# Performance work log

Measured on AMD Instinct MI355X. Metric: run time of the kernel, lower is better.

## Reference

```python
import jax, jax.numpy as jnp
import numpy as np

N = 16384  # n_nodes
D = 64     # feature dim


def setup_inputs() -> dict:
    key = jax.random.key(0)
    kx, ka = jax.random.split(key)
    x = jax.random.normal(kx, (N, D), dtype=jnp.float32)
    # original code only tests adj[idx] == 1, so 0/1 int entries are faithful
    adj = jax.random.randint(ka, (N, N), 0, 2, dtype=jnp.int32)
    return {"x": x, "adj": adj}


def reference(x, adj):
    # GraphPool: for each node, sum its own feature vector plus the feature
    # vectors of all neighbors j with adj[i, j] == 1.
    # Vectorized: out = adj @ x + x  (dense binary SpMM + self term).
    a = (adj == 1).astype(x.dtype)  # [N, N]
    return jnp.matmul(a, x) + x     # [N, D]
```

## Files before the change

kernel.cpp:

```cpp
#include <hip/hip_runtime.h>

#define NN 16384
#define DD 64

typedef _Float16 f16x8 __attribute__((ext_vector_type(8)));
typedef short    s16x8 __attribute__((ext_vector_type(8)));
typedef float    f32x4 __attribute__((ext_vector_type(4)));
typedef int      i32x4 __attribute__((ext_vector_type(4)));

__global__ __launch_bounds__(256) void prep_x(const float* __restrict__ x,
                                              _Float16* __restrict__ ws) {
    __shared__ float sx[32][65];
    const int tid = threadIdx.x;
    const int t   = blockIdx.x;

    {
        int r  = tid >> 3;
        int c8 = (tid & 7) * 8;
        const float* src = x + ((size_t)t * 32 + r) * DD + c8;
        f32x4 a = *(const f32x4*)src;
        f32x4 b = *(const f32x4*)(src + 4);
#pragma unroll
        for (int j = 0; j < 4; ++j) { sx[r][c8 + j] = a[j]; sx[r][c8 + 4 + j] = b[j]; }
    }
    __syncthreads();

    const int l = tid & 63;
    const int c = tid >> 6;
    const int q = l >> 4;
    const int m = l & 15;
    f16x8 v;
#pragma unroll
    for (int j = 0; j < 8; ++j)
        v[j] = (_Float16)sx[q * 8 + j][c * 16 + m];
    *(f16x8*)(ws + (((size_t)t * 256 + c * 64 + l) * 8)) = v;
}

__global__ __launch_bounds__(256, 3) void graphpool_gemm(const int* __restrict__ adj,
                                                         const _Float16* __restrict__ xs,
                                                         float* __restrict__ part) {
    __shared__ _Float16 sB[2][8192];

    const int tid = threadIdx.x;
    const int w   = tid >> 6;
    const int l   = tid & 63;
    const int q   = l >> 4;
    const int m   = l & 15;

    const int rb    = blockIdx.x >> 2;
    const int kq    = blockIdx.x & 3;
    const int row16 = rb * 64 + w * 16;
    constexpr int KQ  = NN / 4;
    constexpr int NCH = KQ / 128;

    const int* aptr = adj + (size_t)(row16 + m) * NN + (size_t)kq * KQ + q * 8;

    f32x4 acc[4];
#pragma unroll
    for (int c = 0; c < 4; ++c) acc[c] = (f32x4){0.f, 0.f, 0.f, 0.f};

    i32x4 areg[2][4][2];
    f16x8 sreg[4];

    auto loadA = [&](int n, int buf) {
#pragma unroll
        for (int s = 0; s < 4; ++s) {
            const i32x4* p = (const i32x4*)(aptr + (size_t)n * 128 + s * 32);
            areg[buf][s][0] = __builtin_nontemporal_load(p);
            areg[buf][s][1] = __builtin_nontemporal_load(p + 1);
        }
    };
    auto stageRead = [&](int n) {
        const f16x8* src = (const f16x8*)xs + (size_t)kq * 32768 + (size_t)n * 1024;
#pragma unroll
        for (int p = 0; p < 4; ++p) sreg[p] = src[p * 256 + tid];
    };
    auto stageWrite = [&](int buf) {
        f16x8* dst = (f16x8*)sB[buf];
#pragma unroll
        for (int p = 0; p < 4; ++p) dst[p * 256 + tid] = sreg[p];
    };

    stageRead(0);
    loadA(0, 0);
    stageWrite(0);
    __syncthreads();

    for (int n = 0; n < NCH; ++n) {
        const int buf = n & 1;
        const bool pf = (n + 1 < NCH);
        if (pf) { stageRead(n + 1); loadA(n + 1, buf ^ 1); }
#pragma unroll
        for (int s = 0; s < 4; ++s) {
            int av[8];
            {
                i32x4 v0 = areg[buf][s][0], v1 = areg[buf][s][1];
                av[0] = v0.x; av[1] = v0.y; av[2] = v0.z; av[3] = v0.w;
                av[4] = v1.x; av[5] = v1.y; av[6] = v1.z; av[7] = v1.w;
            }
            s16x8 ai;
#pragma unroll
            for (int j = 0; j < 8; ++j)
                ai[j] = av[j] ? (short)0x3C00 : (short)0;
            f16x8 af = __builtin_bit_cast(f16x8, ai);
#pragma unroll
            for (int c = 0; c < 4; ++c) {
                f16x8 bf = *(const f16x8*)&sB[buf][((s * 4 + c) * 64 + l) * 8];
                acc[c] = __builtin_amdgcn_mfma_f32_16x16x32_f16(af, bf, acc[c], 0, 0, 0);
            }
        }
        if (pf) stageWrite(buf ^ 1);
        __syncthreads();
    }

    float* po = part + (size_t)kq * NN * DD;
#pragma unroll
    for (int c = 0; c < 4; ++c) {
#pragma unroll
        for (int r = 0; r < 4; ++r) {
            size_t off = (size_t)(row16 + q * 4 + r) * DD + c * 16 + m;
            po[off] = acc[c][r];
        }
    }
}

__global__ __launch_bounds__(256) void reduce_add(const float* __restrict__ part,
                                                  const float* __restrict__ x,
                                                  float* __restrict__ out) {
    size_t i = (size_t)blockIdx.x * 256 + threadIdx.x;
    f32x4 v = ((const f32x4*)x)[i];
#pragma unroll
    for (int g = 0; g < 4; ++g)
        v += ((const f32x4*)(part + (size_t)g * NN * DD))[i];
    ((f32x4*)out)[i] = v;
}

__global__ void graphpool_fallback(const int* __restrict__ adj,
                                   const float* __restrict__ x,
                                   float* __restrict__ out) {
    int i = blockIdx.x;
    int d = threadIdx.x;
    float acc = x[(size_t)i * DD + d];
    const int* row = adj + (size_t)i * NN;
    for (int j = 0; j < NN; ++j)
        if (row[j]) acc += x[(size_t)j * DD + d];
    out[(size_t)i * DD + d] = acc;
}

extern "C" void kernel_launch(void* const* d_in, const int* in_sizes, int n_in,
                              void* d_out, int out_size, void* d_ws, size_t ws_size,
                              hipStream_t stream) {
    const float* x   = (const float*)d_in[0];
    const int*   adj = (const int*)d_in[1];
    float*       out = (float*)d_out;

    const size_t xs_bytes   = (size_t)NN * DD * sizeof(_Float16);
    const size_t part_bytes = (size_t)4 * NN * DD * sizeof(float);
    if (ws_size >= xs_bytes + part_bytes) {
        _Float16* xs   = (_Float16*)d_ws;
        float*    part = (float*)((char*)d_ws + xs_bytes);
        prep_x<<<512, 256, 0, stream>>>(x, xs);
        graphpool_gemm<<<1024, 256, 0, stream>>>(adj, xs, part);
        reduce_add<<<1024, 256, 0, stream>>>(part, x, out);
    } else {
        graphpool_fallback<<<NN, 64, 0, stream>>>(adj, x, out);
    }
}
```

Measured before the change: 1.695 ms.

## Bit-pack adjacency in a prep pass and fuse self-add into single-pass GEMM

```diff
diff --git a/kernel.cpp b/kernel.cpp
--- a/kernel.cpp
+++ b/kernel.cpp
@@ -7,13 +7,32 @@
 typedef short    s16x8 __attribute__((ext_vector_type(8)));
 typedef float    f32x4 __attribute__((ext_vector_type(4)));
 typedef int      i32x4 __attribute__((ext_vector_type(4)));
+typedef unsigned u32;
+
+__global__ __launch_bounds__(256) void prep_adj(const int* __restrict__ adj,
+                                                u32* __restrict__ pk) {
+    const u32 tid = blockIdx.x * 256 + threadIdx.x;
+    for (int it = 0; it < 16; ++it) {
+        size_t g = (size_t)it * (2048 * 256) + tid;
+        const i32x4* src = (const i32x4*)(adj + g * 32);
+        u32 b = 0;
+#pragma unroll
+        for (int j = 0; j < 8; ++j) {
+            i32x4 v = __builtin_nontemporal_load(src + j);
+            b |= (u32)(v.x != 0) << (j * 4 + 0);
+            b |= (u32)(v.y != 0) << (j * 4 + 1);
+            b |= (u32)(v.z != 0) << (j * 4 + 2);
+            b |= (u32)(v.w != 0) << (j * 4 + 3);
+        }
+        pk[g] = b;
+    }
+}
 
 __global__ __launch_bounds__(256) void prep_x(const float* __restrict__ x,
                                               _Float16* __restrict__ ws) {
     __shared__ float sx[32][65];
     const int tid = threadIdx.x;
     const int t   = blockIdx.x;
-
     {
         int r  = tid >> 3;
         int c8 = (tid & 7) * 8;
@@ -24,7 +43,6 @@
         for (int j = 0; j < 4; ++j) { sx[r][c8 + j] = a[j]; sx[r][c8 + 4 + j] = b[j]; }
     }
     __syncthreads();
-
     const int l = tid & 63;
     const int c = tid >> 6;
     const int q = l >> 4;
@@ -36,9 +54,10 @@
     *(f16x8*)(ws + (((size_t)t * 256 + c * 64 + l) * 8)) = v;
 }
 
-__global__ __launch_bounds__(256, 3) void graphpool_gemm(const int* __restrict__ adj,
-                                                         const _Float16* __restrict__ xs,
-                                                         float* __restrict__ part) {
+__global__ __launch_bounds__(256) void graphpool_gemm(const u32* __restrict__ pk,
+                                                      const float* __restrict__ x,
+                                                      const _Float16* __restrict__ xs,
+                                                      float* __restrict__ out) {
     __shared__ _Float16 sB[2][8192];
 
     const int tid = threadIdx.x;
@@ -46,32 +65,20 @@
     const int l   = tid & 63;
     const int q   = l >> 4;
     const int m   = l & 15;
+    const int row16 = blockIdx.x * 64 + w * 16;
 
-    const int rb    = blockIdx.x >> 2;
-    const int kq    = blockIdx.x & 3;
-    const int row16 = rb * 64 + w * 16;
-    constexpr int KQ  = NN / 4;
-    constexpr int NCH = KQ / 128;
-
-    const int* aptr = adj + (size_t)(row16 + m) * NN + (size_t)kq * KQ + q * 8;
+    const i32x4* aptr = (const i32x4*)pk + (size_t)(row16 + m) * 128;
 
     f32x4 acc[4];
 #pragma unroll
     for (int c = 0; c < 4; ++c) acc[c] = (f32x4){0.f, 0.f, 0.f, 0.f};
 
-    i32x4 areg[2][4][2];
+    i32x4 areg[2];
     f16x8 sreg[4];
 
-    auto loadA = [&](int n, int buf) {
-#pragma unroll
-        for (int s = 0; s < 4; ++s) {
-            const i32x4* p = (const i32x4*)(aptr + (size_t)n * 128 + s * 32);
-            areg[buf][s][0] = __builtin_nontemporal_load(p);
-            areg[buf][s][1] = __builtin_nontemporal_load(p + 1);
-        }
-    };
+    auto loadA = [&](int n, int buf) { areg[buf] = aptr[n]; };
     auto stageRead = [&](int n) {
-        const f16x8* src = (const f16x8*)xs + (size_t)kq * 32768 + (size_t)n * 1024;
+        const f16x8* src = (const f16x8*)xs + (size_t)n * 1024;
 #pragma unroll
         for (int p = 0; p < 4; ++p) sreg[p] = src[p * 256 + tid];
     };
@@ -86,22 +93,18 @@
     stageWrite(0);
     __syncthreads();
 
+    constexpr int NCH = NN / 128;
     for (int n = 0; n < NCH; ++n) {
         const int buf = n & 1;
         const bool pf = (n + 1 < NCH);
         if (pf) { stageRead(n + 1); loadA(n + 1, buf ^ 1); }
 #pragma unroll
         for (int s = 0; s < 4; ++s) {
-            int av[8];
-            {
-                i32x4 v0 = areg[buf][s][0], v1 = areg[buf][s][1];
-                av[0] = v0.x; av[1] = v0.y; av[2] = v0.z; av[3] = v0.w;
-                av[4] = v1.x; av[5] = v1.y; av[6] = v1.z; av[7] = v1.w;
-            }
+            u32 byte = (((u32)areg[buf][s]) >> (q * 8)) & 0xffu;
             s16x8 ai;
 #pragma unroll
             for (int j = 0; j < 8; ++j)
-                ai[j] = av[j] ? (short)0x3C00 : (short)0;
+                ai[j] = ((byte >> j) & 1u) ? (short)0x3C00 : (short)0;
             f16x8 af = __builtin_bit_cast(f16x8, ai);
 #pragma unroll
             for (int c = 0; c < 4; ++c) {
@@ -113,26 +116,16 @@
         __syncthreads();
     }
 
-    float* po = part + (size_t)kq * NN * DD;
 #pragma unroll
     for (int c = 0; c < 4; ++c) {
 #pragma unroll
         for (int r = 0; r < 4; ++r) {
-            size_t off = (size_t)(row16 + q * 4 + r) * DD + c * 16 + m;
-            po[off] = acc[c][r];
+            int row = row16 + q * 4 + r;
+            int col = c * 16 + m;
+            size_t off = (size_t)row * DD + col;
+            out[off] = acc[c][r] + x[off];
         }
     }
-}
-
-__global__ __launch_bounds__(256) void reduce_add(const float* __restrict__ part,
-                                                  const float* __restrict__ x,
-                                                  float* __restrict__ out) {
-    size_t i = (size_t)blockIdx.x * 256 + threadIdx.x;
-    f32x4 v = ((const f32x4*)x)[i];
-#pragma unroll
-    for (int g = 0; g < 4; ++g)
-        v += ((const f32x4*)(part + (size_t)g * NN * DD))[i];
-    ((f32x4*)out)[i] = v;
 }
 
 __global__ void graphpool_fallback(const int* __restrict__ adj,
@@ -154,14 +147,14 @@
     const int*   adj = (const int*)d_in[1];
     float*       out = (float*)d_out;
 
-    const size_t xs_bytes   = (size_t)NN * DD * sizeof(_Float16);
-    const size_t part_bytes = (size_t)4 * NN * DD * sizeof(float);
-    if (ws_size >= xs_bytes + part_bytes) {
-        _Float16* xs   = (_Float16*)d_ws;
-        float*    part = (float*)((char*)d_ws + xs_bytes);
+    const size_t xs_bytes = (size_t)NN * DD * sizeof(_Float16);
+    const size_t pk_bytes = (size_t)NN * (NN / 32) * sizeof(u32);
+    if (ws_size >= xs_bytes + pk_bytes) {
+        _Float16* xs = (_Float16*)d_ws;
+        u32*      pk = (u32*)((char*)d_ws + xs_bytes);
+        prep_adj<<<2048, 256, 0, stream>>>(adj, pk);
         prep_x<<<512, 256, 0, stream>>>(x, xs);
-        graphpool_gemm<<<1024, 256, 0, stream>>>(adj, xs, part);
-        reduce_add<<<1024, 256, 0, stream>>>(part, x, out);
+        graphpool_gemm<<<256, 256, 0, stream>>>(pk, x, xs, out);
     } else {
         graphpool_fallback<<<NN, 64, 0, stream>>>(adj, x, out);
     }
```

After: 1.681 ms. Within noise of the previous version (-0.8%).

## Coalesce adjacency loads row-wise, ballot-pack into LDS bitmasks, halve K split

Applied to the files above, without the earlier changes.

```diff
diff --git a/kernel.cpp b/kernel.cpp
--- a/kernel.cpp
+++ b/kernel.cpp
@@ -7,13 +7,15 @@
 typedef short    s16x8 __attribute__((ext_vector_type(8)));
 typedef float    f32x4 __attribute__((ext_vector_type(4)));
 typedef int      i32x4 __attribute__((ext_vector_type(4)));
+typedef int      i32x2 __attribute__((ext_vector_type(2)));
+typedef unsigned u32;
+typedef unsigned long long u64;
 
 __global__ __launch_bounds__(256) void prep_x(const float* __restrict__ x,
                                               _Float16* __restrict__ ws) {
     __shared__ float sx[32][65];
     const int tid = threadIdx.x;
     const int t   = blockIdx.x;
-
     {
         int r  = tid >> 3;
         int c8 = (tid & 7) * 8;
@@ -24,7 +26,6 @@
         for (int j = 0; j < 4; ++j) { sx[r][c8 + j] = a[j]; sx[r][c8 + 4 + j] = b[j]; }
     }
     __syncthreads();
-
     const int l = tid & 63;
     const int c = tid >> 6;
     const int q = l >> 4;
@@ -40,6 +41,7 @@
                                                          const _Float16* __restrict__ xs,
                                                          float* __restrict__ part) {
     __shared__ _Float16 sB[2][8192];
+    __shared__ u32      sA[2][256];
 
     const int tid = threadIdx.x;
     const int w   = tid >> 6;
@@ -47,31 +49,45 @@
     const int q   = l >> 4;
     const int m   = l & 15;
 
-    const int rb    = blockIdx.x >> 2;
-    const int kq    = blockIdx.x & 3;
+    const int rb    = blockIdx.x >> 1;
+    const int kq    = blockIdx.x & 1;
     const int row16 = rb * 64 + w * 16;
-    constexpr int KQ  = NN / 4;
-    constexpr int NCH = KQ / 128;
+    constexpr int KH  = NN / 2;
+    constexpr int NCH = KH / 128;
 
-    const int* aptr = adj + (size_t)(row16 + m) * NN + (size_t)kq * KQ + q * 8;
+    const int* abase = adj + (size_t)row16 * NN + (size_t)kq * KH;
 
     f32x4 acc[4];
 #pragma unroll
     for (int c = 0; c < 4; ++c) acc[c] = (f32x4){0.f, 0.f, 0.f, 0.f};
 
-    i32x4 areg[2][4][2];
+    i32x2 areg[16];
     f16x8 sreg[4];
 
-    auto loadA = [&](int n, int buf) {
+    auto loadAdj = [&](int n) {
 #pragma unroll
-        for (int s = 0; s < 4; ++s) {
-            const i32x4* p = (const i32x4*)(aptr + (size_t)n * 128 + s * 32);
-            areg[buf][s][0] = __builtin_nontemporal_load(p);
-            areg[buf][s][1] = __builtin_nontemporal_load(p + 1);
+        for (int rr = 0; rr < 16; ++rr) {
+            const i32x2* p = (const i32x2*)(abase + (size_t)rr * NN + n * 128);
+            areg[rr] = p[l];
         }
     };
+    auto packA = [&](int buf) {
+        u32 mine = 0;
+#pragma unroll
+        for (int rr = 0; rr < 16; ++rr) {
+            u64 b0 = __ballot(areg[rr].x != 0);
+            u64 b1 = __ballot(areg[rr].y != 0);
+            u32 lo0 = (u32)b0, hi0 = (u32)(b0 >> 32);
+            u32 lo1 = (u32)b1, hi1 = (u32)(b1 >> 32);
+            u32 sa  = (l & 1) ? hi0 : lo0;
+            u32 sb  = (l & 1) ? hi1 : lo1;
+            u32 sel = (l & 2) ? sb : sa;
+            if ((l >> 2) == rr) mine = sel;
+        }
+        sA[buf][w * 64 + l] = mine;
+    };
     auto stageRead = [&](int n) {
-        const f16x8* src = (const f16x8*)xs + (size_t)kq * 32768 + (size_t)n * 1024;
+        const f16x8* src = (const f16x8*)xs + ((size_t)kq * NCH + n) * 1024;
 #pragma unroll
         for (int p = 0; p < 4; ++p) sreg[p] = src[p * 256 + tid];
     };
@@ -81,27 +97,29 @@
         for (int p = 0; p < 4; ++p) dst[p * 256 + tid] = sreg[p];
     };
 
+    loadAdj(0);
     stageRead(0);
-    loadA(0, 0);
+    packA(0);
     stageWrite(0);
     __syncthreads();
 
     for (int n = 0; n < NCH; ++n) {
         const int buf = n & 1;
         const bool pf = (n + 1 < NCH);
-        if (pf) { stageRead(n + 1); loadA(n + 1, buf ^ 1); }
+        if (pf) { loadAdj(n + 1); stageRead(n + 1); }
+
+        i32x4 rowAi = *(const i32x4*)&sA[buf][(w * 16 + m) * 4];
 #pragma unroll
         for (int s = 0; s < 4; ++s) {
-            int av[8];
-            {
-                i32x4 v0 = areg[buf][s][0], v1 = areg[buf][s][1];
-                av[0] = v0.x; av[1] = v0.y; av[2] = v0.z; av[3] = v0.w;
-                av[4] = v1.x; av[5] = v1.y; av[6] = v1.z; av[7] = v1.w;
-            }
+            const u32 bq = 16 * (s & 1) + 4 * q;
+            const u32 dE = (u32)rowAi[s >> 1];
+            const u32 dO = (u32)rowAi[2 + (s >> 1)];
             s16x8 ai;
 #pragma unroll
-            for (int j = 0; j < 8; ++j)
-                ai[j] = av[j] ? (short)0x3C00 : (short)0;
+            for (int j = 0; j < 8; ++j) {
+                u32 d = (j & 1) ? dO : dE;
+                ai[j] = ((d >> (bq + (j >> 1))) & 1u) ? (short)0x3C00 : (short)0;
+            }
             f16x8 af = __builtin_bit_cast(f16x8, ai);
 #pragma unroll
             for (int c = 0; c < 4; ++c) {
@@ -109,7 +127,8 @@
                 acc[c] = __builtin_amdgcn_mfma_f32_16x16x32_f16(af, bf, acc[c], 0, 0, 0);
             }
         }
-        if (pf) stageWrite(buf ^ 1);
+
+        if (pf) { packA(buf ^ 1); stageWrite(buf ^ 1); }
         __syncthreads();
     }
 
@@ -129,9 +148,8 @@
                                                   float* __restrict__ out) {
     size_t i = (size_t)blockIdx.x * 256 + threadIdx.x;
     f32x4 v = ((const f32x4*)x)[i];
-#pragma unroll
-    for (int g = 0; g < 4; ++g)
-        v += ((const f32x4*)(part + (size_t)g * NN * DD))[i];
+    v += ((const f32x4*)part)[i];
+    v += ((const f32x4*)(part + (size_t)NN * DD))[i];
     ((f32x4*)out)[i] = v;
 }
 
@@ -155,12 +173,12 @@
     float*       out = (float*)d_out;
 
     const size_t xs_bytes   = (size_t)NN * DD * sizeof(_Float16);
-    const size_t part_bytes = (size_t)4 * NN * DD * sizeof(float);
+    const size_t part_bytes = (size_t)2 * NN * DD * sizeof(float);
     if (ws_size >= xs_bytes + part_bytes) {
         _Float16* xs   = (_Float16*)d_ws;
         float*    part = (float*)((char*)d_ws + xs_bytes);
         prep_x<<<512, 256, 0, stream>>>(x, xs);
-        graphpool_gemm<<<1024, 256, 0, stream>>>(adj, xs, part);
+        graphpool_gemm<<<512, 256, 0, stream>>>(adj, xs, part);
         reduce_add<<<1024, 256, 0, stream>>>(part, x, out);
     } else {
         graphpool_fallback<<<NN, 64, 0, stream>>>(adj, x, out);
```

After: 1.388 ms. -18.1%, faster.
